# Performance work log

Hardware: AMD Instinct MI355X
Metric: run time of the kernel (lower is better)

Reference implementation:

```python
import jax, jax.numpy as jnp
import numpy as np

N_CHANNEL = 64
N_BAND = 5
N_CLASS = 2
B = 64
K = 2 * N_CHANNEL  # nodes covered by the fully-connected edge_index


def _w(key, shape):
    fan_in = shape[0] if len(shape) == 2 else int(np.prod(shape[1:]))
    return (jax.random.normal(key, shape, jnp.float32) / np.float32(np.sqrt(fan_in)))


def setup_inputs() -> dict:
    key = jax.random.key(0)
    ks = jax.random.split(key, 22)
    d = {}
    d['x1'] = jax.random.normal(ks[0], (B, K, N_BAND), jnp.float32)
    d['x2'] = jax.random.normal(ks[1], (B, K, K), jnp.float32)
    # GCNConv params (weights stored (in, out); PyG applies linear then aggregates, bias after)
    d['gcn1_w'] = _w(ks[2], (N_BAND, 2 * N_BAND))
    d['gcn1_b'] = 0.01 * jax.random.normal(ks[3], (2 * N_BAND,), jnp.float32)
    d['gcn2_w'] = _w(ks[4], (2 * N_BAND, 1))
    d['gcn2_b'] = 0.01 * jax.random.normal(ks[5], (1,), jnp.float32)
    d['fcg_w'] = _w(ks[6], (K, K))
    d['fcg_b'] = 0.01 * jax.random.normal(ks[7], (K,), jnp.float32)
    d['conv1_w'] = _w(ks[8], (16, 1, 3, 3))   # OIHW
    d['conv1_b'] = 0.01 * jax.random.normal(ks[9], (16,), jnp.float32)
    d['conv2_w'] = _w(ks[10], (16, 16, 3, 3))
    d['conv2_b'] = 0.01 * jax.random.normal(ks[11], (16,), jnp.float32)
    d['fcc_w'] = _w(ks[12], (16 * K * K, K))
    d['fcc_b'] = 0.01 * jax.random.normal(ks[13], (K,), jnp.float32)
    d['fc1_w'] = _w(ks[14], (4 * N_CHANNEL, 2 * N_CHANNEL))
    d['fc1_b'] = 0.01 * jax.random.normal(ks[15], (2 * N_CHANNEL,), jnp.float32)
    d['fc2_w'] = _w(ks[16], (2 * N_CHANNEL, N_CHANNEL))
    d['fc2_b'] = 0.01 * jax.random.normal(ks[17], (N_CHANNEL,), jnp.float32)
    d['fc3_w'] = _w(ks[18], (N_CHANNEL, N_CLASS))
    d['fc3_b'] = 0.01 * jax.random.normal(ks[19], (N_CLASS,), jnp.float32)
    return d


def _gcn(x, W, b):
    # Faithful to original: edge_index is fully connected over the FIRST K rows only.
    # With default self-loops, normalized adjacency over rows [0,K) is (1/K)*ones(K,K)
    # (all degrees = K); every other row has only its self-loop (degree 1 -> identity).
    y = x @ W                                   # (B*N, out)
    y = y.at[:K].set(jnp.mean(y[:K], axis=0))   # broadcast mean over first K rows
    return y + b


def _conv(x, w, b):
    y = jax.lax.conv_general_dilated(x, w, (1, 1), 'SAME',
                                     dimension_numbers=('NCHW', 'OIHW', 'NCHW'))
    return jax.nn.relu(y + b[None, :, None, None])


def reference(x1, x2, gcn1_w, gcn1_b, gcn2_w, gcn2_b, fcg_w, fcg_b,
              conv1_w, conv1_b, conv2_w, conv2_b, fcc_w, fcc_b,
              fc1_w, fc1_b, fc2_w, fc2_b, fc3_w, fc3_b):
    Bn, N, Feat = x1.shape
    # GNN branch (dropout is identity in eval mode)
    h = x1.reshape(Bn * N, Feat)
    h = jax.nn.relu(_gcn(h, gcn1_w, gcn1_b))
    h = jax.nn.relu(_gcn(h, gcn2_w, gcn2_b))
    h = h.reshape(Bn, -1)                       # (B, 2*n_channel)
    g = jax.nn.relu(h @ fcg_w + fcg_b)
    # CNN branch
    c = x2[:, None]                             # (B,1,H,W)
    c = _conv(c, conv1_w, conv1_b)
    c = _conv(c, conv2_w, conv2_b)
    c = c.reshape(Bn, -1)                       # channel-major flatten, same as torch .view
    c = jax.nn.relu(c @ fcc_w + fcc_b)
    # Fusion MLP
    x = jnp.concatenate([c, g], axis=1)
    x = jax.nn.relu(x @ fc1_w + fc1_b)
    x = jax.nn.relu(x @ fc2_w + fc2_b)
    return jax.nn.sigmoid(x @ fc3_w + fc3_b)
```

## Files before the change

kernel.cpp:

```cpp
#include <hip/hip_runtime.h>
#include <hip/hip_bf16.h>


#define IMG     16384
#define FCC_K   262144
#define FCC_BLOCKS 1024
#define FCC_KRANGE 256
#define FCC_CHUNK 64
#define FCC_NCHUNK 4

typedef __attribute__((ext_vector_type(8))) short bf16x8;
typedef __attribute__((ext_vector_type(4))) float f32x4;
typedef __attribute__((ext_vector_type(4))) unsigned short us4;
typedef __attribute__((ext_vector_type(8))) unsigned short us8;

__device__ __forceinline__ unsigned short f2bf(float f) {
    unsigned u = __float_as_uint(f);
    unsigned r = (u + 0x7FFFu + ((u >> 16) & 1u)) >> 16;
    return (unsigned short)r;
}
__device__ __forceinline__ float bf2f(unsigned short b) {
    unsigned u = ((unsigned)b) << 16;
    return __uint_as_float(u);
}

__device__ __forceinline__ int fcc_swz64(int col, int k) {
    return col*64 + (k ^ ((((col >> 2) ^ col) & 7) << 3));
}

__global__ __launch_bounds__(256) void conv12_kernel(
    const float* __restrict__ x2,
    const float* __restrict__ w1,
    const float* __restrict__ b1,
    const float* __restrict__ w2,
    const float* __restrict__ b2,
    unsigned short* __restrict__ c2bf)
{
    __shared__ float sx2[8][130];
    __shared__ unsigned short sin[6*130*16];
    __shared__ unsigned short sB[5*512];
    __shared__ float sw1[144], sb1v[16];

    int tid = threadIdx.x;
    int blk = blockIdx.x;
    int b   = blk >> 5;
    int R0  = (blk & 31) * 4;

    if (tid < 144) sw1[tid] = w1[tid];
    if (tid < 16)  sb1v[tid] = b1[tid];

    for (int idx = tid; idx < 2560; idx += 256) {
        int q   = idx >> 9;
        int rem = idx & 511;
        int l   = rem >> 3;
        int e   = rem & 7;
        int k   = (l >> 4) * 8 + e;
        int oc  = l & 15;
        int ic  = k & 15;
        int dd  = 2*q + (k >> 4);
        unsigned short bits = 0;
        if (dd < 9) bits = f2bf(w2[oc*144 + ic*9 + dd]);
        sB[idx] = bits;
    }
    if (tid < 192) {
        int rr = tid >> 5, rem = tid & 31;
        int cc = (rem < 16) ? 0 : 129;
        sin[(rr*130 + cc)*16 + (rem & 15)] = 0;
    }
    {
        const float* xb = x2 + (size_t)b * IMG;
        for (int idx = tid; idx < 8*130; idx += 256) {
            int rr = idx / 130, cc = idx - rr*130;
            int ri = R0 - 2 + rr, gj = cc - 1;
            float v = 0.f;
            if (ri >= 0 && ri < 128 && gj >= 0 && gj < 128)
                v = xb[ri*128 + gj];
            sx2[rr][cc] = v;
        }
    }
    __syncthreads();

    for (int p = tid; p < 768; p += 256) {
        int rr = p >> 7;
        int cc = p & 127;
        int ri1 = R0 - 1 + rr;
        bool valid = (ri1 >= 0 && ri1 < 128);
        float in9[3][3];
        #pragma unroll
        for (int di = 0; di < 3; ++di)
          #pragma unroll
          for (int dj = 0; dj < 3; ++dj)
              in9[di][dj] = sx2[rr + di][cc + dj];
        us8 o0, o1;
        #pragma unroll
        for (int oc = 0; oc < 16; ++oc) {
            float acc = sb1v[oc];
            #pragma unroll
            for (int di = 0; di < 3; ++di)
              #pragma unroll
              for (int dj = 0; dj < 3; ++dj)
                  acc += in9[di][dj] * sw1[oc*9 + di*3 + dj];
            unsigned short bits = valid ? f2bf(fmaxf(acc, 0.f)) : (unsigned short)0;
            if (oc < 8) o0[oc] = bits; else o1[oc - 8] = bits;
        }
        unsigned short* dst = &sin[(rr*130 + cc + 1)*16];
        *reinterpret_cast<us8*>(dst)     = o0;
        *reinterpret_cast<us8*>(dst + 8) = o1;
    }
    __syncthreads();

    int lane = tid & 63;
    int wv   = tid >> 6;
    int ln   = lane & 15;
    int g    = lane >> 4;
    int ghalf = g & 1;

    int aoff[5];
    #pragma unroll
    for (int q = 0; q < 5; ++q) {
        int dd = 2*q + (g >> 1);
        if (dd > 8) dd = 8;
        int di = dd / 3, dj = dd % 3;
        aoff[q] = ((wv + di)*130 + ln + dj)*16 + ghalf*8;
    }

    bf16x8 bf[5];
    #pragma unroll
    for (int q = 0; q < 5; ++q)
        bf[q] = *reinterpret_cast<const bf16x8*>(&sB[q*512 + lane*8]);

    float bias_oc = b2[ln];
    int r = R0 + wv;
    unsigned short* outbase = c2bf + ((size_t)b*16 + ln)*IMG + r*128;

    #pragma unroll
    for (int t = 0; t < 8; ++t) {
        f32x4 acc = {0.f, 0.f, 0.f, 0.f};
        #pragma unroll
        for (int q = 0; q < 5; ++q) {
            bf16x8 a = *reinterpret_cast<const bf16x8*>(&sin[aoff[q] + t*256]);
            acc = __builtin_amdgcn_mfma_f32_16x16x32_bf16(a, bf[q], acc, 0, 0, 0);
        }
        int pc = t*16 + g*4;
        us4 pk;
        #pragma unroll
        for (int reg = 0; reg < 4; ++reg)
            pk[reg] = f2bf(fmaxf(acc[reg] + bias_oc, 0.f));
        *reinterpret_cast<us4*>(&outbase[pc]) = pk;
    }
}

__global__ __launch_bounds__(256, 4) void fcc_mfma(
    const unsigned short* __restrict__ c2bf,
    const float* __restrict__ W,
    unsigned short* __restrict__ partials)
{
    __shared__ unsigned short sWt[FCC_CHUNK*128];

    int tid  = threadIdx.x;
    int blk  = blockIdx.x;
    int k0   = blk * FCC_KRANGE;
    int lane = tid & 63, wv = tid >> 6;
    int ln   = lane & 15, g = lane >> 4;
    int q    = tid & 31;
    int kO   = tid >> 5;
    int col0 = q*4;

    f32x4 acc[8];
    #pragma unroll
    for (int j = 0; j < 8; ++j) acc[j] = (f32x4){0.f,0.f,0.f,0.f};

    const float* Wb = W + (size_t)k0 * 128;
    const unsigned short* arow = c2bf + (size_t)(16*wv + ln)*FCC_K + k0 + g*8;

    for (int ci = 0; ci < FCC_NCHUNK; ++ci) {
        const float* Wc = Wb + (size_t)ci * FCC_CHUNK * 128;
        float4 rows[8];
        #pragma unroll
        for (int r = 0; r < 8; ++r)
            rows[r] = *reinterpret_cast<const float4*>(
                Wc + (size_t)(kO*8 + r)*128 + col0);
        {
            us8 vc0, vc1, vc2, vc3;
            #pragma unroll
            for (int r = 0; r < 8; ++r) {
                vc0[r] = f2bf(rows[r].x); vc1[r] = f2bf(rows[r].y);
                vc2[r] = f2bf(rows[r].z); vc3[r] = f2bf(rows[r].w);
            }
            *reinterpret_cast<us8*>(&sWt[fcc_swz64(col0+0, kO*8)]) = vc0;
            *reinterpret_cast<us8*>(&sWt[fcc_swz64(col0+1, kO*8)]) = vc1;
            *reinterpret_cast<us8*>(&sWt[fcc_swz64(col0+2, kO*8)]) = vc2;
            *reinterpret_cast<us8*>(&sWt[fcc_swz64(col0+3, kO*8)]) = vc3;
        }
        __syncthreads();

        bf16x8 af0 = *reinterpret_cast<const bf16x8*>(arow + ci*FCC_CHUNK);
        bf16x8 af1 = *reinterpret_cast<const bf16x8*>(arow + ci*FCC_CHUNK + 32);
        #pragma unroll
        for (int j = 0; j < 8; ++j) {
            bf16x8 bfrag = *reinterpret_cast<const bf16x8*>(
                &sWt[fcc_swz64(j*16 + ln, g*8)]);
            acc[j] = __builtin_amdgcn_mfma_f32_16x16x32_bf16(af0, bfrag, acc[j], 0, 0, 0);
        }
        #pragma unroll
        for (int j = 0; j < 8; ++j) {
            bf16x8 bfrag = *reinterpret_cast<const bf16x8*>(
                &sWt[fcc_swz64(j*16 + ln, 32 + g*8)]);
            acc[j] = __builtin_amdgcn_mfma_f32_16x16x32_bf16(af1, bfrag, acc[j], 0, 0, 0);
        }
        __syncthreads();
    }

    unsigned short* p = partials + (size_t)blk * 8192;
    #pragma unroll
    for (int j = 0; j < 8; ++j)
      #pragma unroll
      for (int reg = 0; reg < 4; ++reg) {
          int m = 16*wv + g*4 + reg;
          p[m*128 + j*16 + ln] = f2bf(acc[j][reg]);
      }
}

__global__ __launch_bounds__(256) void fcc_reduce(
    const unsigned short* __restrict__ partials,
    const float* __restrict__ bias,
    float* __restrict__ cvec)
{
    __shared__ float sred[8][32];
    int blk = blockIdx.x, t = threadIdx.x;
    int o  = blk*32 + (t & 31);
    int pr = t >> 5;
    const unsigned short* pb = partials + (size_t)pr*8192 + o;
    float s = 0.f;
    #pragma unroll 16
    for (int i = 0; i < FCC_BLOCKS/8; ++i)
        s += bf2f(pb[(size_t)i*8*8192]);
    sred[pr][t & 31] = s;
    __syncthreads();
    if (t < 32) {
        float v = 0.f;
        #pragma unroll
        for (int p2 = 0; p2 < 8; ++p2) v += sred[p2][t];
        cvec[o] = fmaxf(v + bias[o & 127], 0.f);
    }
}

__global__ __launch_bounds__(128) void head_kernel(
    const float* __restrict__ cvec,
    const float* __restrict__ x1,
    const float* __restrict__ gW1, const float* __restrict__ gb1,
    const float* __restrict__ gW2, const float* __restrict__ gb2,
    const float* __restrict__ fcgW, const float* __restrict__ fcgb,
    const float* __restrict__ w1, const float* __restrict__ bb1,
    const float* __restrict__ w2, const float* __restrict__ bb2,
    const float* __restrict__ w3, const float* __restrict__ bb3,
    float* __restrict__ out)
{
    __shared__ float sx[256], sh[128], s2[64], sh2[128];
    __shared__ float sW1[50], sb1s[10], sW2s[10], smean[10];
    __shared__ float sy1[128][10];
    int b = blockIdx.x, t = threadIdx.x;

    if (t < 50) sW1[t] = gW1[t];
    if (t >= 64 && t < 74) { sb1s[t-64] = gb1[t-64]; sW2s[t-64] = gW2[t-64]; }
    sx[t] = cvec[b*128 + t];
    __syncthreads();

    float y[10];
    {
        int r = b*128 + t;
        float x[5];
        #pragma unroll
        for (int f = 0; f < 5; ++f) x[f] = x1[r*5 + f];
        #pragma unroll
        for (int oo = 0; oo < 10; ++oo) {
            float a = 0.f;
            #pragma unroll
            for (int f = 0; f < 5; ++f) a += x[f] * sW1[f*10 + oo];
            y[oo] = a;
        }
    }
    if (b == 0) {
        #pragma unroll
        for (int oo = 0; oo < 10; ++oo) sy1[t][oo] = y[oo];
        __syncthreads();
        if (t < 10) {
            float s = 0.f;
            for (int rr = 0; rr < 128; ++rr) s += sy1[rr][t];
            smean[t] = fmaxf(s * (1.f/128.f) + sb1s[t], 0.f);
        }
        __syncthreads();
    }
    {
        float h1row[10];
        if (b == 0) {
            #pragma unroll
            for (int oo = 0; oo < 10; ++oo) h1row[oo] = smean[oo];
        } else {
            #pragma unroll
            for (int oo = 0; oo < 10; ++oo) h1row[oo] = fmaxf(y[oo] + sb1s[oo], 0.f);
        }
        float y2 = 0.f;
        #pragma unroll
        for (int oo = 0; oo < 10; ++oo) y2 += h1row[oo] * sW2s[oo];
        sh2[t] = fmaxf(y2 + gb2[0], 0.f);
    }
    __syncthreads();

    {
        float acc = fcgb[t];
        #pragma unroll 8
        for (int k = 0; k < 128; ++k) acc += sh2[k] * fcgW[k*128 + t];
        sx[128 + t] = fmaxf(acc, 0.f);
    }
    __syncthreads();

    {
        float acc = bb1[t];
        for (int k = 0; k < 256; ++k) acc += sx[k] * w1[k*128 + t];
        sh[t] = fmaxf(acc, 0.f);
    }
    __syncthreads();
    if (t < 64) {
        float acc = bb2[t];
        for (int k = 0; k < 128; ++k) acc += sh[k] * w2[k*64 + t];
        s2[t] = fmaxf(acc, 0.f);
    }
    __syncthreads();
    if (t < 2) {
        float acc = bb3[t];
        for (int k = 0; k < 64; ++k) acc += s2[k] * w3[k*2 + t];
        out[b*2 + t] = 1.f / (1.f + __expf(-acc));
    }
}

extern "C" void kernel_launch(void* const* d_in, const int* in_sizes, int n_in,
                              void* d_out, int out_size, void* d_ws, size_t ws_size,
                              hipStream_t stream)
{
    const float* x1      = (const float*)d_in[0];
    const float* x2      = (const float*)d_in[1];
    const float* gcn1_w  = (const float*)d_in[2];
    const float* gcn1_b  = (const float*)d_in[3];
    const float* gcn2_w  = (const float*)d_in[4];
    const float* gcn2_b  = (const float*)d_in[5];
    const float* fcg_w   = (const float*)d_in[6];
    const float* fcg_b   = (const float*)d_in[7];
    const float* conv1_w = (const float*)d_in[8];
    const float* conv1_b = (const float*)d_in[9];
    const float* conv2_w = (const float*)d_in[10];
    const float* conv2_b = (const float*)d_in[11];
    const float* fcc_w   = (const float*)d_in[12];
    const float* fcc_b   = (const float*)d_in[13];
    const float* fc1_w   = (const float*)d_in[14];
    const float* fc1_b   = (const float*)d_in[15];
    const float* fc2_w   = (const float*)d_in[16];
    const float* fc2_b   = (const float*)d_in[17];
    const float* fc3_w   = (const float*)d_in[18];
    const float* fc3_b   = (const float*)d_in[19];
    float* out = (float*)d_out;

    unsigned short* c2bf     = (unsigned short*)d_ws;
    unsigned short* partials = c2bf + 16777216;
    float* cvec = (float*)(partials + 8388608);

    conv12_kernel<<<2048, 256, 0, stream>>>(x2, conv1_w, conv1_b,
                                            conv2_w, conv2_b, c2bf);
    fcc_mfma<<<FCC_BLOCKS, 256, 0, stream>>>(c2bf, fcc_w, partials);
    fcc_reduce<<<256, 256, 0, stream>>>(partials, fcc_b, cvec);
    head_kernel<<<64, 128, 0, stream>>>(cvec, x1, gcn1_w, gcn1_b,
                                        gcn2_w, gcn2_b, fcg_w, fcg_b,
                                        fc1_w, fc1_b, fc2_w, fc2_b,
                                        fc3_w, fc3_b, out);
}
```

Measured before the change: 96.49 us.

## Load FCC weights directly into MFMA B fragments, dropping LDS staging

The fcc_mfma kernel no longer stages fp32 weight chunks through swizzled shared memory. Each lane now reads its eight fp32 weights straight from global memory in MFMA fragment order, packs them to bf16 in registers, and issues the MFMA. This removes LDS traffic and both __syncthreads per chunk. The cost is that every one of the four waves reads the full weight tile independently, giving 4x redundant global/L2 reads with scalar, strided loads. Rounding also changes to a cheaper round-half-up bf16 pack.

```diff
diff --git a/kernel.cpp b/kernel.cpp
--- a/kernel.cpp
+++ b/kernel.cpp
@@ -6,13 +6,12 @@
 #define FCC_K   262144
 #define FCC_BLOCKS 1024
 #define FCC_KRANGE 256
-#define FCC_CHUNK 64
-#define FCC_NCHUNK 4
 
 typedef __attribute__((ext_vector_type(8))) short bf16x8;
 typedef __attribute__((ext_vector_type(4))) float f32x4;
 typedef __attribute__((ext_vector_type(4))) unsigned short us4;
 typedef __attribute__((ext_vector_type(8))) unsigned short us8;
+typedef __attribute__((ext_vector_type(4))) unsigned int u32x4;
 
 __device__ __forceinline__ unsigned short f2bf(float f) {
     unsigned u = __float_as_uint(f);
@@ -23,9 +22,10 @@
     unsigned u = ((unsigned)b) << 16;
     return __uint_as_float(u);
 }
-
-__device__ __forceinline__ int fcc_swz64(int col, int k) {
-    return col*64 + (k ^ ((((col >> 2) ^ col) & 7) << 3));
+__device__ __forceinline__ unsigned pack2bf(float a, float b) {
+    unsigned ua = __float_as_uint(a) + 0x8000u;
+    unsigned ub = __float_as_uint(b) + 0x8000u;
+    return (ua >> 16) | (ub & 0xFFFF0000u);
 }
 
 __global__ __launch_bounds__(256) void conv12_kernel(
@@ -155,60 +155,36 @@
     const float* __restrict__ W,
     unsigned short* __restrict__ partials)
 {
-    __shared__ unsigned short sWt[FCC_CHUNK*128];
-
     int tid  = threadIdx.x;
     int blk  = blockIdx.x;
     int k0   = blk * FCC_KRANGE;
     int lane = tid & 63, wv = tid >> 6;
     int ln   = lane & 15, g = lane >> 4;
-    int q    = tid & 31;
-    int kO   = tid >> 5;
-    int col0 = q*4;
 
     f32x4 acc[8];
     #pragma unroll
     for (int j = 0; j < 8; ++j) acc[j] = (f32x4){0.f,0.f,0.f,0.f};
 
-    const float* Wb = W + (size_t)k0 * 128;
     const unsigned short* arow = c2bf + (size_t)(16*wv + ln)*FCC_K + k0 + g*8;
 
-    for (int ci = 0; ci < FCC_NCHUNK; ++ci) {
-        const float* Wc = Wb + (size_t)ci * FCC_CHUNK * 128;
-        float4 rows[8];
-        #pragma unroll
-        for (int r = 0; r < 8; ++r)
-            rows[r] = *reinterpret_cast<const float4*>(
-                Wc + (size_t)(kO*8 + r)*128 + col0);
-        {
-            us8 vc0, vc1, vc2, vc3;
-            #pragma unroll
-            for (int r = 0; r < 8; ++r) {
-                vc0[r] = f2bf(rows[r].x); vc1[r] = f2bf(rows[r].y);
-                vc2[r] = f2bf(rows[r].z); vc3[r] = f2bf(rows[r].w);
-            }
-            *reinterpret_cast<us8*>(&sWt[fcc_swz64(col0+0, kO*8)]) = vc0;
-            *reinterpret_cast<us8*>(&sWt[fcc_swz64(col0+1, kO*8)]) = vc1;
-            *reinterpret_cast<us8*>(&sWt[fcc_swz64(col0+2, kO*8)]) = vc2;
-            *reinterpret_cast<us8*>(&sWt[fcc_swz64(col0+3, kO*8)]) = vc3;
-        }
-        __syncthreads();
-
-        bf16x8 af0 = *reinterpret_cast<const bf16x8*>(arow + ci*FCC_CHUNK);
-        bf16x8 af1 = *reinterpret_cast<const bf16x8*>(arow + ci*FCC_CHUNK + 32);
+    for (int ks = 0; ks < 8; ++ks) {
+        bf16x8 af = *reinterpret_cast<const bf16x8*>(arow + ks*32);
+        const float* Wk = W + (size_t)(k0 + ks*32 + g*8)*128 + ln;
         #pragma unroll
         for (int j = 0; j < 8; ++j) {
-            bf16x8 bfrag = *reinterpret_cast<const bf16x8*>(
-                &sWt[fcc_swz64(j*16 + ln, g*8)]);
-            acc[j] = __builtin_amdgcn_mfma_f32_16x16x32_bf16(af0, bfrag, acc[j], 0, 0, 0);
-        }
-        #pragma unroll
-        for (int j = 0; j < 8; ++j) {
-            bf16x8 bfrag = *reinterpret_cast<const bf16x8*>(
-                &sWt[fcc_swz64(j*16 + ln, 32 + g*8)]);
-            acc[j] = __builtin_amdgcn_mfma_f32_16x16x32_bf16(af1, bfrag, acc[j], 0, 0, 0);
-        }
-        __syncthreads();
+            const float* Wj = Wk + j*16;
+            float w0 = Wj[0*128], w1 = Wj[1*128];
+            float w2 = Wj[2*128], w3 = Wj[3*128];
+            float w4 = Wj[4*128], w5 = Wj[5*128];
+            float w6 = Wj[6*128], w7 = Wj[7*128];
+            u32x4 pk;
+            pk[0] = pack2bf(w0, w1);
+            pk[1] = pack2bf(w2, w3);
+            pk[2] = pack2bf(w4, w5);
+            pk[3] = pack2bf(w6, w7);
+            bf16x8 bfrag = *reinterpret_cast<bf16x8*>(&pk);
+            acc[j] = __builtin_amdgcn_mfma_f32_16x16x32_bf16(af, bfrag, acc[j], 0, 0, 0);
+        }
     }
 
     unsigned short* p = partials + (size_t)blk * 8192;
```

Result: slower. 98.84 us (+2.4%).
